# Optimization experiments

Measured on AMD Instinct MI355X. Metric: run time of the kernel, lower is better.

## Reference

```python
import jax, jax.numpy as jnp
import numpy as np

K, M, N = 8, 1024, 1024  # bits, in_features, out_features (nf)
B_, S_ = 4, 2048

def setup_inputs() -> dict:
    key = jax.random.key(0)
    k1, k2, k3, k4 = jax.random.split(key, 4)
    x = jax.random.normal(k1, (B_, S_, M), dtype=jnp.float32)
    # per-bit +/-1 sign matrices, stored as float (module casts int8 -> x.dtype)
    binary = jnp.where(jax.random.normal(k2, (K, M, N)) > 0, 1.0, -1.0).astype(jnp.float32)
    # positive per-bit, per-output-channel scales (sup decomposition yields positives)
    scale = jax.random.uniform(k3, (K, 1, N), dtype=jnp.float32, minval=0.01, maxval=1.0)
    bias = jax.random.normal(k4, (N,), dtype=jnp.float32)
    return {"x": x, "binary": binary, "scale": scale, "bias": bias}

def reference(x, binary, scale, bias):
    size_out = x.shape[:-1] + (N,)
    x2 = x.reshape(-1, x.shape[-1])                 # [T, m]
    # k separate dense matmuls against +/-1 matrices: [k, T, n]
    xk = jnp.einsum('tm,kmn->ktn', x2, binary)
    out = jnp.sum(xk * scale, axis=0)               # per-bit scale then sum over bits
    out = out + bias
    return out.reshape(size_out)
```

## Files before the change

kernel.cpp:

```cpp
#include <hip/hip_runtime.h>
#include <cstdint>

#define TDIM 8192
#define MDIM 1024
#define NDIM 1024
#define KBITS 8
#define BK 64
#define BT 128
#define BN 128
#define NTILES (MDIM / BK)

typedef __bf16 bf16x8 __attribute__((ext_vector_type(8)));
typedef float f32x4 __attribute__((ext_vector_type(4)));

#define GAS(p) ((__attribute__((address_space(1))) void*)(uintptr_t)(p))
#define LAS(p) ((__attribute__((address_space(3))) void*)(uintptr_t)(p))

__device__ __forceinline__ unsigned short f2bf(float f) {
    union { float f; unsigned u; } v; v.f = f;
    unsigned r = v.u + 0x7fffu + ((v.u >> 16) & 1u);
    return (unsigned short)(r >> 16);
}

__global__ __launch_bounds__(256) void prep_kernel(const float* __restrict__ x,
                                                   unsigned short* __restrict__ xb,
                                                   const float* __restrict__ binary,
                                                   const float* __restrict__ scale,
                                                   unsigned short* __restrict__ wtr) {
    __shared__ float tile[32][33];
    const int tid = threadIdx.x;
    if (blockIdx.x >= 1024) {
        size_t idx = ((size_t)(blockIdx.x - 1024) * 256 + tid) * 8;
        float4 a = *(const float4*)(x + idx);
        float4 b = *(const float4*)(x + idx + 4);
        uint4 o;
        o.x = (unsigned)f2bf(a.x) | ((unsigned)f2bf(a.y) << 16);
        o.y = (unsigned)f2bf(a.z) | ((unsigned)f2bf(a.w) << 16);
        o.z = (unsigned)f2bf(b.x) | ((unsigned)f2bf(b.y) << 16);
        o.w = (unsigned)f2bf(b.z) | ((unsigned)f2bf(b.w) << 16);
        *(uint4*)(xb + idx) = o;
        return;
    }
    const int n0 = (blockIdx.x & 31) * 32;
    const int m0 = (blockIdx.x >> 5) * 32;
    const int r = tid >> 3;
    const int cn = (tid & 7) * 4;
    f32x4 acc = {0.f, 0.f, 0.f, 0.f};
#pragma unroll
    for (int k = 0; k < KBITS; ++k) {
        f32x4 v = *(const f32x4*)(binary + ((size_t)k * MDIM + m0 + r) * NDIM + n0 + cn);
        f32x4 s = *(const f32x4*)(scale + (size_t)k * NDIM + n0 + cn);
        acc += v * s;
    }
#pragma unroll
    for (int e = 0; e < 4; ++e) tile[cn + e][r] = acc[e];
    __syncthreads();
    const int rn = tid >> 3;
    const int cm = (tid & 7) * 4;
    ushort4 o4;
    o4.x = f2bf(tile[rn][cm + 0]);
    o4.y = f2bf(tile[rn][cm + 1]);
    o4.z = f2bf(tile[rn][cm + 2]);
    o4.w = f2bf(tile[rn][cm + 3]);
    *(ushort4*)(wtr + (size_t)(n0 + rn) * MDIM + m0 + cm) = o4;
}

__global__ __launch_bounds__(256, 2) void gemm_kernel(const unsigned short* __restrict__ xb,
                                                      const unsigned short* __restrict__ wtr,
                                                      const float* __restrict__ bias,
                                                      float* __restrict__ out) {
    constexpr int ASZ = BT * BK;
    constexpr int BSZ = BN * BK;
    constexpr int BUF = ASZ + BSZ;
    __shared__ __attribute__((aligned(16))) unsigned short lds[2 * BUF];

    const int tid = threadIdx.x;
    const int lane = tid & 63;
    const int wv = tid >> 6;
    const int wm = wv >> 1;
    const int wn = wv & 1;
    const int lrow = lane & 15;
    const int q = lane >> 4;

    const int t0 = blockIdx.x * BT;
    const int n0 = blockIdx.y * BN;

    const unsigned short* srcA[4];
    int dstA[4];
    const unsigned short* srcB[4];
    int dstB[4];
#pragma unroll
    for (int j = 0; j < 4; ++j) {
        int s = tid + j * 256;
        int r = s >> 3;
        int g = (s & 7) ^ (r & 7);
        srcA[j] = xb + (size_t)(t0 + r) * MDIM + g * 8;
        dstA[j] = s * 8;
        srcB[j] = wtr + (size_t)(n0 + r) * MDIM + g * 8;
        dstB[j] = ASZ + s * 8;
    }

    int a_off[2][4], b_off[2][4];
#pragma unroll
    for (int h = 0; h < 2; ++h)
#pragma unroll
        for (int i = 0; i < 4; ++i) {
            int m = wm * 64 + i * 16 + lrow;
            a_off[h][i] = (m * 8 + ((h * 4 + q) ^ (m & 7))) * 8;
            int n = wn * 64 + i * 16 + lrow;
            b_off[h][i] = ASZ + (n * 8 + ((h * 4 + q) ^ (n & 7))) * 8;
        }

    f32x4 acc[4][4];
    const f32x4 zero = {0.f, 0.f, 0.f, 0.f};
#pragma unroll
    for (int i = 0; i < 4; ++i)
#pragma unroll
        for (int j = 0; j < 4; ++j) acc[i][j] = zero;

    auto stage = [&](int bufsel, int t) {
        unsigned short* bb = lds + bufsel * BUF;
        const int k0 = t * BK;
#pragma unroll
        for (int j = 0; j < 4; ++j)
            __builtin_amdgcn_global_load_lds(GAS(srcA[j] + k0), LAS(bb + dstA[j]), 16, 0, 0);
#pragma unroll
        for (int j = 0; j < 4; ++j)
            __builtin_amdgcn_global_load_lds(GAS(srcB[j] + k0), LAS(bb + dstB[j]), 16, 0, 0);
    };

    stage(0, 0);
    __syncthreads();

#pragma unroll
    for (int t = 0; t < NTILES; ++t) {
        const int cur = t & 1;
        if (t + 1 < NTILES) stage(cur ^ 1, t + 1);

        const unsigned short* base = lds + cur * BUF;
#pragma unroll
        for (int h = 0; h < 2; ++h) {
            bf16x8 af[4], bfr[4];
#pragma unroll
            for (int i = 0; i < 4; ++i) af[i] = *(const bf16x8*)(base + a_off[h][i]);
#pragma unroll
            for (int i = 0; i < 4; ++i) bfr[i] = *(const bf16x8*)(base + b_off[h][i]);
            __builtin_amdgcn_s_setprio(1);
#pragma unroll
            for (int i = 0; i < 4; ++i)
#pragma unroll
                for (int j = 0; j < 4; ++j)
                    acc[i][j] = __builtin_amdgcn_mfma_f32_16x16x32_bf16(af[i], bfr[j],
                                                                        acc[i][j], 0, 0, 0);
            __builtin_amdgcn_s_setprio(0);
        }

        if (t + 1 < NTILES) __syncthreads();
    }

#pragma unroll
    for (int j = 0; j < 4; ++j) {
        const int n = n0 + wn * 64 + j * 16 + lrow;
        const float bv = bias[n];
#pragma unroll
        for (int i = 0; i < 4; ++i) {
            const int tb = t0 + wm * 64 + i * 16 + q * 4;
#pragma unroll
            for (int r = 0; r < 4; ++r) {
                out[(size_t)(tb + r) * NDIM + n] = acc[i][j][r] + bv;
            }
        }
    }
}

extern "C" void kernel_launch(void* const* d_in, const int* in_sizes, int n_in,
                              void* d_out, int out_size, void* d_ws, size_t ws_size,
                              hipStream_t stream) {
    const float* x      = (const float*)d_in[0];
    const float* binary = (const float*)d_in[1];
    const float* scale  = (const float*)d_in[2];
    const float* bias   = (const float*)d_in[3];
    float* out = (float*)d_out;

    unsigned short* xb  = (unsigned short*)d_ws;
    unsigned short* wtr = xb + (size_t)TDIM * MDIM;

    prep_kernel<<<1024 + 4096, 256, 0, stream>>>(x, xb, binary, scale, wtr);
    gemm_kernel<<<dim3(TDIM / BT, NDIM / BN), 256, 0, stream>>>(xb, wtr, bias, out);
}
```

Before: 123.1 us.

## Fuse x bf16 conversion into GEMM with per-row-block atomic barrier

Moves the fp32->bf16 conversion of x out of the prep kernel and into the GEMM kernel. Each of the 8 N-blocks sharing a T row-block converts 16 rows, then they synchronise through an atomic counter spin-wait before loading A tiles. This overlaps the conversion with the weight fold and the GEMM launch, and drops most of the prep kernel's work. The spin-wait can deadlock if the 8 blocks of a row group are not co-resident, and it adds synchronisation stalls.

```diff
diff --git a/kernel.cpp b/kernel.cpp
--- a/kernel.cpp
+++ b/kernel.cpp
@@ -22,25 +22,13 @@
     return (unsigned short)(r >> 16);
 }
 
-__global__ __launch_bounds__(256) void prep_kernel(const float* __restrict__ x,
-                                                   unsigned short* __restrict__ xb,
-                                                   const float* __restrict__ binary,
-                                                   const float* __restrict__ scale,
-                                                   unsigned short* __restrict__ wtr) {
+__global__ __launch_bounds__(256) void wfold_kernel(const float* __restrict__ binary,
+                                                    const float* __restrict__ scale,
+                                                    unsigned short* __restrict__ wtr,
+                                                    int* __restrict__ cnt) {
     __shared__ float tile[32][33];
     const int tid = threadIdx.x;
-    if (blockIdx.x >= 1024) {
-        size_t idx = ((size_t)(blockIdx.x - 1024) * 256 + tid) * 8;
-        float4 a = *(const float4*)(x + idx);
-        float4 b = *(const float4*)(x + idx + 4);
-        uint4 o;
-        o.x = (unsigned)f2bf(a.x) | ((unsigned)f2bf(a.y) << 16);
-        o.y = (unsigned)f2bf(a.z) | ((unsigned)f2bf(a.w) << 16);
-        o.z = (unsigned)f2bf(b.x) | ((unsigned)f2bf(b.y) << 16);
-        o.w = (unsigned)f2bf(b.z) | ((unsigned)f2bf(b.w) << 16);
-        *(uint4*)(xb + idx) = o;
-        return;
-    }
+    if (blockIdx.x == 0 && tid < 64) cnt[tid] = 0;
     const int n0 = (blockIdx.x & 31) * 32;
     const int m0 = (blockIdx.x >> 5) * 32;
     const int r = tid >> 3;
@@ -65,10 +53,12 @@
     *(ushort4*)(wtr + (size_t)(n0 + rn) * MDIM + m0 + cm) = o4;
 }
 
-__global__ __launch_bounds__(256, 2) void gemm_kernel(const unsigned short* __restrict__ xb,
+__global__ __launch_bounds__(256, 2) void gemm_kernel(const float* __restrict__ x,
+                                                      unsigned short* __restrict__ xb,
                                                       const unsigned short* __restrict__ wtr,
                                                       const float* __restrict__ bias,
-                                                      float* __restrict__ out) {
+                                                      float* __restrict__ out,
+                                                      int* __restrict__ cnt) {
     constexpr int ASZ = BT * BK;
     constexpr int BSZ = BN * BK;
     constexpr int BUF = ASZ + BSZ;
@@ -84,6 +74,25 @@
 
     const int t0 = blockIdx.x * BT;
     const int n0 = blockIdx.y * BN;
+
+    {
+        const int row0 = t0 + blockIdx.y * 16;
+#pragma unroll 4
+        for (int i = 0; i < 16; ++i) {
+            float4 a = *(const float4*)(x + (size_t)(row0 + i) * MDIM + tid * 4);
+            ushort4 o;
+            o.x = f2bf(a.x); o.y = f2bf(a.y); o.z = f2bf(a.z); o.w = f2bf(a.w);
+            *(ushort4*)(xb + (size_t)(row0 + i) * MDIM + tid * 4) = o;
+        }
+    }
+    __syncthreads();
+    if (tid == 0)
+        __hip_atomic_fetch_add(&cnt[blockIdx.x], 1, __ATOMIC_RELEASE,
+                               __HIP_MEMORY_SCOPE_AGENT);
+    while (__hip_atomic_load(&cnt[blockIdx.x], __ATOMIC_ACQUIRE,
+                             __HIP_MEMORY_SCOPE_AGENT) < 8)
+        __builtin_amdgcn_s_sleep(4);
+    __syncthreads();
 
     const unsigned short* srcA[4];
     int dstA[4];
@@ -184,7 +193,8 @@
 
     unsigned short* xb  = (unsigned short*)d_ws;
     unsigned short* wtr = xb + (size_t)TDIM * MDIM;
-
-    prep_kernel<<<1024 + 4096, 256, 0, stream>>>(x, xb, binary, scale, wtr);
-    gemm_kernel<<<dim3(TDIM / BT, NDIM / BN), 256, 0, stream>>>(xb, wtr, bias, out);
-}
+    int* cnt = (int*)(wtr + (size_t)NDIM * MDIM);
+
+    wfold_kernel<<<1024, 256, 0, stream>>>(binary, scale, wtr, cnt);
+    gemm_kernel<<<dim3(TDIM / BT, NDIM / BN), 256, 0, stream>>>(x, xb, wtr, bias, out, cnt);
+}
```

Result: slower. 221.3 us (+79.8%).

## Pre-pack operands into MFMA fragment layout and load directly from global

Applied to the files above, without the earlier changes.

The prep kernel now writes x and the folded weight in a blocked layout that matches the MFMA fragment order: 16-row tiles, grouped by 8 elements along the reduction dimension. The GEMM drops LDS staging, double buffering and barriers, and each wave loads its bf16x8 fragments straight from global memory with coalesced 16-byte loads. The aim is to remove LDS traffic and synchronisation overhead. In exchange, operands are no longer shared through LDS, so each wave rereads its tiles from L2/global, and global latency is hidden only by unrolling and occupancy rather than explicit prefetch.

```diff
diff --git a/kernel.cpp b/kernel.cpp
--- a/kernel.cpp
+++ b/kernel.cpp
@@ -5,42 +5,47 @@
 #define MDIM 1024
 #define NDIM 1024
 #define KBITS 8
-#define BK 64
 #define BT 128
 #define BN 128
-#define NTILES (MDIM / BK)
 
 typedef __bf16 bf16x8 __attribute__((ext_vector_type(8)));
 typedef float f32x4 __attribute__((ext_vector_type(4)));
 
-#define GAS(p) ((__attribute__((address_space(1))) void*)(uintptr_t)(p))
-#define LAS(p) ((__attribute__((address_space(3))) void*)(uintptr_t)(p))
-
-__device__ __forceinline__ unsigned short f2bf(float f) {
+__device__ __forceinline__ unsigned f2bf(float f) {
     union { float f; unsigned u; } v; v.f = f;
     unsigned r = v.u + 0x7fffu + ((v.u >> 16) & 1u);
-    return (unsigned short)(r >> 16);
+    return r >> 16;
 }
 
+
 __global__ __launch_bounds__(256) void prep_kernel(const float* __restrict__ x,
-                                                   unsigned short* __restrict__ xb,
+                                                   unsigned short* __restrict__ xbp,
                                                    const float* __restrict__ binary,
                                                    const float* __restrict__ scale,
-                                                   unsigned short* __restrict__ wtr) {
-    __shared__ float tile[32][33];
+                                                   unsigned short* __restrict__ wtrp) {
     const int tid = threadIdx.x;
     if (blockIdx.x >= 1024) {
-        size_t idx = ((size_t)(blockIdx.x - 1024) * 256 + tid) * 8;
-        float4 a = *(const float4*)(x + idx);
-        float4 b = *(const float4*)(x + idx + 4);
-        uint4 o;
-        o.x = (unsigned)f2bf(a.x) | ((unsigned)f2bf(a.y) << 16);
-        o.y = (unsigned)f2bf(a.z) | ((unsigned)f2bf(a.w) << 16);
-        o.z = (unsigned)f2bf(b.x) | ((unsigned)f2bf(b.y) << 16);
-        o.w = (unsigned)f2bf(b.z) | ((unsigned)f2bf(b.w) << 16);
-        *(uint4*)(xb + idx) = o;
+        const int b = blockIdx.x - 1024;
+        const float* src = x + (size_t)b * 16 * MDIM;
+        unsigned short* dst = xbp + (size_t)b * 16384;
+#pragma unroll
+        for (int p = 0; p < 8; ++p) {
+            int s = p * 256 + tid;
+            int r16 = s >> 7;
+            int g = s & 127;
+            const float* sp = src + (size_t)r16 * MDIM + g * 8;
+            float4 a = *(const float4*)sp;
+            float4 c = *(const float4*)(sp + 4);
+            uint4 o;
+            o.x = f2bf(a.x) | (f2bf(a.y) << 16);
+            o.y = f2bf(a.z) | (f2bf(a.w) << 16);
+            o.z = f2bf(c.x) | (f2bf(c.y) << 16);
+            o.w = f2bf(c.z) | (f2bf(c.w) << 16);
+            *(uint4*)(dst + (size_t)g * 128 + r16 * 8) = o;
+        }
         return;
     }
+    __shared__ float tile[32][33];
     const int n0 = (blockIdx.x & 31) * 32;
     const int m0 = (blockIdx.x >> 5) * 32;
     const int r = tid >> 3;
@@ -57,23 +62,20 @@
     __syncthreads();
     const int rn = tid >> 3;
     const int cm = (tid & 7) * 4;
+    const int n = n0 + rn;
+    const int m = m0 + cm;
     ushort4 o4;
-    o4.x = f2bf(tile[rn][cm + 0]);
-    o4.y = f2bf(tile[rn][cm + 1]);
-    o4.z = f2bf(tile[rn][cm + 2]);
-    o4.w = f2bf(tile[rn][cm + 3]);
-    *(ushort4*)(wtr + (size_t)(n0 + rn) * MDIM + m0 + cm) = o4;
+    o4.x = (unsigned short)f2bf(tile[rn][cm + 0]);
+    o4.y = (unsigned short)f2bf(tile[rn][cm + 1]);
+    o4.z = (unsigned short)f2bf(tile[rn][cm + 2]);
+    o4.w = (unsigned short)f2bf(tile[rn][cm + 3]);
+    *(ushort4*)(wtrp + ((size_t)(n >> 4) * 128 + (m >> 3)) * 128 + (n & 15) * 8 + (m & 7)) = o4;
 }
 
-__global__ __launch_bounds__(256, 2) void gemm_kernel(const unsigned short* __restrict__ xb,
-                                                      const unsigned short* __restrict__ wtr,
+__global__ __launch_bounds__(256, 2) void gemm_kernel(const unsigned short* __restrict__ xbp,
+                                                      const unsigned short* __restrict__ wtrp,
                                                       const float* __restrict__ bias,
                                                       float* __restrict__ out) {
-    constexpr int ASZ = BT * BK;
-    constexpr int BSZ = BN * BK;
-    constexpr int BUF = ASZ + BSZ;
-    __shared__ __attribute__((aligned(16))) unsigned short lds[2 * BUF];
-
     const int tid = threadIdx.x;
     const int lane = tid & 63;
     const int wv = tid >> 6;
@@ -82,34 +84,16 @@
     const int lrow = lane & 15;
     const int q = lane >> 4;
 
-    const int t0 = blockIdx.x * BT;
-    const int n0 = blockIdx.y * BN;
+    const int tt0 = blockIdx.x * (BT / 16);
+    const int nt0 = blockIdx.y * (BN / 16);
 
-    const unsigned short* srcA[4];
-    int dstA[4];
-    const unsigned short* srcB[4];
-    int dstB[4];
+    const unsigned short* abase[4];
+    const unsigned short* bbase[4];
 #pragma unroll
-    for (int j = 0; j < 4; ++j) {
-        int s = tid + j * 256;
-        int r = s >> 3;
-        int g = (s & 7) ^ (r & 7);
-        srcA[j] = xb + (size_t)(t0 + r) * MDIM + g * 8;
-        dstA[j] = s * 8;
-        srcB[j] = wtr + (size_t)(n0 + r) * MDIM + g * 8;
-        dstB[j] = ASZ + s * 8;
+    for (int i = 0; i < 4; ++i) {
+        abase[i] = xbp + (size_t)(tt0 + wm * 4 + i) * 16384 + q * 128 + lrow * 8;
+        bbase[i] = wtrp + (size_t)(nt0 + wn * 4 + i) * 16384 + q * 128 + lrow * 8;
     }
-
-    int a_off[2][4], b_off[2][4];
-#pragma unroll
-    for (int h = 0; h < 2; ++h)
-#pragma unroll
-        for (int i = 0; i < 4; ++i) {
-            int m = wm * 64 + i * 16 + lrow;
-            a_off[h][i] = (m * 8 + ((h * 4 + q) ^ (m & 7))) * 8;
-            int n = wn * 64 + i * 16 + lrow;
-            b_off[h][i] = ASZ + (n * 8 + ((h * 4 + q) ^ (n & 7))) * 8;
-        }
 
     f32x4 acc[4][4];
     const f32x4 zero = {0.f, 0.f, 0.f, 0.f};
@@ -118,46 +102,24 @@
 #pragma unroll
         for (int j = 0; j < 4; ++j) acc[i][j] = zero;
 
-    auto stage = [&](int bufsel, int t) {
-        unsigned short* bb = lds + bufsel * BUF;
-        const int k0 = t * BK;
+#pragma unroll 4
+    for (int ks = 0; ks < 32; ++ks) {
+        const int off = ks * 512;
+        bf16x8 af[4], bfr[4];
 #pragma unroll
-        for (int j = 0; j < 4; ++j)
-            __builtin_amdgcn_global_load_lds(GAS(srcA[j] + k0), LAS(bb + dstA[j]), 16, 0, 0);
+        for (int i = 0; i < 4; ++i) af[i] = *(const bf16x8*)(abase[i] + off);
 #pragma unroll
-        for (int j = 0; j < 4; ++j)
-            __builtin_amdgcn_global_load_lds(GAS(srcB[j] + k0), LAS(bb + dstB[j]), 16, 0, 0);
-    };
-
-    stage(0, 0);
-    __syncthreads();
-
+        for (int i = 0; i < 4; ++i) bfr[i] = *(const bf16x8*)(bbase[i] + off);
 #pragma unroll
-    for (int t = 0; t < NTILES; ++t) {
-        const int cur = t & 1;
-        if (t + 1 < NTILES) stage(cur ^ 1, t + 1);
-
-        const unsigned short* base = lds + cur * BUF;
+        for (int i = 0; i < 4; ++i)
 #pragma unroll
-        for (int h = 0; h < 2; ++h) {
-            bf16x8 af[4], bfr[4];
-#pragma unroll
-            for (int i = 0; i < 4; ++i) af[i] = *(const bf16x8*)(base + a_off[h][i]);
-#pragma unroll
-            for (int i = 0; i < 4; ++i) bfr[i] = *(const bf16x8*)(base + b_off[h][i]);
-            __builtin_amdgcn_s_setprio(1);
-#pragma unroll
-            for (int i = 0; i < 4; ++i)
-#pragma unroll
-                for (int j = 0; j < 4; ++j)
-                    acc[i][j] = __builtin_amdgcn_mfma_f32_16x16x32_bf16(af[i], bfr[j],
-                                                                        acc[i][j], 0, 0, 0);
-            __builtin_amdgcn_s_setprio(0);
-        }
-
-        if (t + 1 < NTILES) __syncthreads();
+            for (int j = 0; j < 4; ++j)
+                acc[i][j] = __builtin_amdgcn_mfma_f32_16x16x32_bf16(af[i], bfr[j],
+                                                                    acc[i][j], 0, 0, 0);
     }
 
+    const int t0 = blockIdx.x * BT;
+    const int n0 = blockIdx.y * BN;
 #pragma unroll
     for (int j = 0; j < 4; ++j) {
         const int n = n0 + wn * 64 + j * 16 + lrow;
@@ -182,9 +144,9 @@
     const float* bias   = (const float*)d_in[3];
     float* out = (float*)d_out;
 
-    unsigned short* xb  = (unsigned short*)d_ws;
-    unsigned short* wtr = xb + (size_t)TDIM * MDIM;
+    unsigned short* xbp  = (unsigned short*)d_ws;
+    unsigned short* wtrp = xbp + (size_t)TDIM * MDIM;
 
-    prep_kernel<<<1024 + 4096, 256, 0, stream>>>(x, xb, binary, scale, wtr);
-    gemm_kernel<<<dim3(TDIM / BT, NDIM / BN), 256, 0, stream>>>(xb, wtr, bias, out);
+    prep_kernel<<<1024 + TDIM / 16, 256, 0, stream>>>(x, xbp, binary, scale, wtrp);
+    gemm_kernel<<<dim3(TDIM / BT, NDIM / BN), 256, 0, stream>>>(xbp, wtrp, bias, out);
 }
```

Measured after the change: 131.3 us. 1.07x slower.

## Pre-pack weights in MFMA fragment order and load B directly into registers

Applied to the files above, without the earlier changes.

The prep kernel now writes the folded bf16 weight matrix in a layout blocked by MFMA fragment (16 n-rows by 8 k-columns), so each lane's B operand sits at a contiguous 16-byte address. The GEMM stops staging B through LDS and reads B fragments straight from global memory into registers, which halves the LDS footprint and allows launch bounds of 3 blocks per CU. The cost is that B loads are no longer shared across the two waves in the same wn column, so more global/L2 traffic is spent, and global load latency now sits in the main loop without explicit prefetch.

```diff
diff --git a/kernel.cpp b/kernel.cpp
--- a/kernel.cpp
+++ b/kernel.cpp
@@ -16,17 +16,17 @@
 #define GAS(p) ((__attribute__((address_space(1))) void*)(uintptr_t)(p))
 #define LAS(p) ((__attribute__((address_space(3))) void*)(uintptr_t)(p))
 
-__device__ __forceinline__ unsigned short f2bf(float f) {
+__device__ __forceinline__ unsigned f2bf(float f) {
     union { float f; unsigned u; } v; v.f = f;
     unsigned r = v.u + 0x7fffu + ((v.u >> 16) & 1u);
-    return (unsigned short)(r >> 16);
+    return r >> 16;
 }
 
 __global__ __launch_bounds__(256) void prep_kernel(const float* __restrict__ x,
                                                    unsigned short* __restrict__ xb,
                                                    const float* __restrict__ binary,
                                                    const float* __restrict__ scale,
-                                                   unsigned short* __restrict__ wtr) {
+                                                   unsigned short* __restrict__ wtrp) {
     __shared__ float tile[32][33];
     const int tid = threadIdx.x;
     if (blockIdx.x >= 1024) {
@@ -34,10 +34,10 @@
         float4 a = *(const float4*)(x + idx);
         float4 b = *(const float4*)(x + idx + 4);
         uint4 o;
-        o.x = (unsigned)f2bf(a.x) | ((unsigned)f2bf(a.y) << 16);
-        o.y = (unsigned)f2bf(a.z) | ((unsigned)f2bf(a.w) << 16);
-        o.z = (unsigned)f2bf(b.x) | ((unsigned)f2bf(b.y) << 16);
-        o.w = (unsigned)f2bf(b.z) | ((unsigned)f2bf(b.w) << 16);
+        o.x = f2bf(a.x) | (f2bf(a.y) << 16);
+        o.y = f2bf(a.z) | (f2bf(a.w) << 16);
+        o.z = f2bf(b.x) | (f2bf(b.y) << 16);
+        o.w = f2bf(b.z) | (f2bf(b.w) << 16);
         *(uint4*)(xb + idx) = o;
         return;
     }
@@ -57,22 +57,22 @@
     __syncthreads();
     const int rn = tid >> 3;
     const int cm = (tid & 7) * 4;
+    const int n = n0 + rn;
+    const int m = m0 + cm;
     ushort4 o4;
-    o4.x = f2bf(tile[rn][cm + 0]);
-    o4.y = f2bf(tile[rn][cm + 1]);
-    o4.z = f2bf(tile[rn][cm + 2]);
-    o4.w = f2bf(tile[rn][cm + 3]);
-    *(ushort4*)(wtr + (size_t)(n0 + rn) * MDIM + m0 + cm) = o4;
+    o4.x = (unsigned short)f2bf(tile[rn][cm + 0]);
+    o4.y = (unsigned short)f2bf(tile[rn][cm + 1]);
+    o4.z = (unsigned short)f2bf(tile[rn][cm + 2]);
+    o4.w = (unsigned short)f2bf(tile[rn][cm + 3]);
+    *(ushort4*)(wtrp + ((size_t)(n >> 4) * 128 + (m >> 3)) * 128 + (n & 15) * 8 + (m & 7)) = o4;
 }
 
-__global__ __launch_bounds__(256, 2) void gemm_kernel(const unsigned short* __restrict__ xb,
-                                                      const unsigned short* __restrict__ wtr,
+__global__ __launch_bounds__(256, 3) void gemm_kernel(const unsigned short* __restrict__ xb,
+                                                      const unsigned short* __restrict__ wtrp,
                                                       const float* __restrict__ bias,
                                                       float* __restrict__ out) {
     constexpr int ASZ = BT * BK;
-    constexpr int BSZ = BN * BK;
-    constexpr int BUF = ASZ + BSZ;
-    __shared__ __attribute__((aligned(16))) unsigned short lds[2 * BUF];
+    __shared__ __attribute__((aligned(16))) unsigned short lds[2 * ASZ];
 
     const int tid = threadIdx.x;
     const int lane = tid & 63;
@@ -84,11 +84,10 @@
 
     const int t0 = blockIdx.x * BT;
     const int n0 = blockIdx.y * BN;
+    const int nt0 = blockIdx.y * (BN / 16);
 
     const unsigned short* srcA[4];
     int dstA[4];
-    const unsigned short* srcB[4];
-    int dstB[4];
 #pragma unroll
     for (int j = 0; j < 4; ++j) {
         int s = tid + j * 256;
@@ -96,20 +95,21 @@
         int g = (s & 7) ^ (r & 7);
         srcA[j] = xb + (size_t)(t0 + r) * MDIM + g * 8;
         dstA[j] = s * 8;
-        srcB[j] = wtr + (size_t)(n0 + r) * MDIM + g * 8;
-        dstB[j] = ASZ + s * 8;
     }
 
-    int a_off[2][4], b_off[2][4];
+    int a_off[2][4];
 #pragma unroll
     for (int h = 0; h < 2; ++h)
 #pragma unroll
         for (int i = 0; i < 4; ++i) {
             int m = wm * 64 + i * 16 + lrow;
             a_off[h][i] = (m * 8 + ((h * 4 + q) ^ (m & 7))) * 8;
-            int n = wn * 64 + i * 16 + lrow;
-            b_off[h][i] = ASZ + (n * 8 + ((h * 4 + q) ^ (n & 7))) * 8;
         }
+
+    const unsigned short* bbase[4];
+#pragma unroll
+    for (int i = 0; i < 4; ++i)
+        bbase[i] = wtrp + (size_t)(nt0 + wn * 4 + i) * 16384 + q * 128 + lrow * 8;
 
     f32x4 acc[4][4];
     const f32x4 zero = {0.f, 0.f, 0.f, 0.f};
@@ -118,40 +118,42 @@
 #pragma unroll
         for (int j = 0; j < 4; ++j) acc[i][j] = zero;
 
-    auto stage = [&](int bufsel, int t) {
-        unsigned short* bb = lds + bufsel * BUF;
+    auto stageA = [&](int bufsel, int t) {
+        unsigned short* bb = lds + bufsel * ASZ;
         const int k0 = t * BK;
 #pragma unroll
         for (int j = 0; j < 4; ++j)
             __builtin_amdgcn_global_load_lds(GAS(srcA[j] + k0), LAS(bb + dstA[j]), 16, 0, 0);
-#pragma unroll
-        for (int j = 0; j < 4; ++j)
-            __builtin_amdgcn_global_load_lds(GAS(srcB[j] + k0), LAS(bb + dstB[j]), 16, 0, 0);
     };
 
-    stage(0, 0);
+    stageA(0, 0);
     __syncthreads();
 
 #pragma unroll
     for (int t = 0; t < NTILES; ++t) {
         const int cur = t & 1;
-        if (t + 1 < NTILES) stage(cur ^ 1, t + 1);
 
-        const unsigned short* base = lds + cur * BUF;
+        bf16x8 bfr0[4], bfr1[4];
+#pragma unroll
+        for (int i = 0; i < 4; ++i) bfr0[i] = *(const bf16x8*)(bbase[i] + (t * 2 + 0) * 512);
+#pragma unroll
+        for (int i = 0; i < 4; ++i) bfr1[i] = *(const bf16x8*)(bbase[i] + (t * 2 + 1) * 512);
+
+        if (t + 1 < NTILES) stageA(cur ^ 1, t + 1);
+
+        const unsigned short* base = lds + cur * ASZ;
 #pragma unroll
         for (int h = 0; h < 2; ++h) {
-            bf16x8 af[4], bfr[4];
+            bf16x8 af[4];
 #pragma unroll
             for (int i = 0; i < 4; ++i) af[i] = *(const bf16x8*)(base + a_off[h][i]);
-#pragma unroll
-            for (int i = 0; i < 4; ++i) bfr[i] = *(const bf16x8*)(base + b_off[h][i]);
             __builtin_amdgcn_s_setprio(1);
 #pragma unroll
             for (int i = 0; i < 4; ++i)
 #pragma unroll
                 for (int j = 0; j < 4; ++j)
-                    acc[i][j] = __builtin_amdgcn_mfma_f32_16x16x32_bf16(af[i], bfr[j],
-                                                                        acc[i][j], 0, 0, 0);
+                    acc[i][j] = __builtin_amdgcn_mfma_f32_16x16x32_bf16(
+                        af[i], (h == 0) ? bfr0[j] : bfr1[j], acc[i][j], 0, 0, 0);
             __builtin_amdgcn_s_setprio(0);
         }
 
@@ -182,9 +184,9 @@
     const float* bias   = (const float*)d_in[3];
     float* out = (float*)d_out;
 
-    unsigned short* xb  = (unsigned short*)d_ws;
-    unsigned short* wtr = xb + (size_t)TDIM * MDIM;
+    unsigned short* xb   = (unsigned short*)d_ws;
+    unsigned short* wtrp = xb + (size_t)TDIM * MDIM;
 
-    prep_kernel<<<1024 + 4096, 256, 0, stream>>>(x, xb, binary, scale, wtr);
-    gemm_kernel<<<dim3(TDIM / BT, NDIM / BN), 256, 0, stream>>>(xb, wtr, bias, out);
+    prep_kernel<<<1024 + 4096, 256, 0, stream>>>(x, xb, binary, scale, wtrp);
+    gemm_kernel<<<dim3(TDIM / BT, NDIM / BN), 256, 0, stream>>>(xb, wtrp, bias, out);
 }
```

Result: no change. 124.7 us (+1.3%).
